# Optimization experiments

Hardware: AMD Instinct MI355X
Metric: run time of the kernel (lower is better)

## Reference

```python
import jax, jax.numpy as jnp
import numpy as np

ALG_DIM = 248   # dim of E8 adjoint rep
NNZ = 30000     # number of nonzero structure constants f_{ij}^k
BATCH = 8192


def setup_inputs() -> dict:
    key = jax.random.key(0)
    k1, k2, k3, k4, k5, k6 = jax.random.split(key, 6)
    x = jax.random.normal(k1, (BATCH, ALG_DIM), dtype=jnp.float32)
    y = jax.random.normal(k2, (BATCH, ALG_DIM), dtype=jnp.float32)
    idx_i = jax.random.randint(k3, (NNZ,), 0, ALG_DIM, dtype=jnp.int32)
    idx_j = jax.random.randint(k4, (NNZ,), 0, ALG_DIM, dtype=jnp.int32)
    idx_k = jax.random.randint(k5, (NNZ,), 0, ALG_DIM, dtype=jnp.int32)
    coeff = jax.random.normal(k6, (NNZ,), dtype=jnp.float32)
    alpha = jnp.ones((1,), dtype=jnp.float32)
    return {"x": x, "y": y, "idx_i": idx_i, "idx_j": idx_j,
            "idx_k": idx_k, "coeff": coeff, "alpha": alpha}


def reference(x, y, idx_i, idx_j, idx_k, coeff, alpha):
    # Sparse Lie bracket via structure-constant triples:
    #   out[b, k] = sum_{t : idx_k[t]==k} coeff[t] * x[b, idx_i[t]] * y[b, idx_j[t]]
    vals = x[:, idx_i] * y[:, idx_j] * coeff[None, :]          # (B, nnz)
    bracket = jnp.zeros_like(x).at[:, idx_k].add(vals)          # (B, 248)
    return alpha[0] * bracket
```

## Files before the change

kernel.cpp:

```cpp
#include <hip/hip_runtime.h>

#define ALG_DIM 248
#define ROWS 32
#define KSPLIT 4
#define KPB 62
#define PMAX 1024
#define CB 32
#define PLSTRIDE_B 3984
#define PLSTRIDE_DW 996

typedef __fp16 h2v __attribute__((ext_vector_type(2)));
union H2U { unsigned u; h2v h; };


__global__ void k_hist(const int* __restrict__ idx_k, int* __restrict__ hist, int nnz) {
    __shared__ int h[256];
    const int b = blockIdx.x, tid = threadIdx.x;
    h[tid] = 0;
    __syncthreads();
    const int chunk = (nnz + CB - 1) / CB;
    const int lo = b * chunk, hi = min(nnz, lo + chunk);
    for (int t = lo + tid; t < hi; t += 256)
        atomicAdd(&h[idx_k[t]], 1);
    __syncthreads();
    hist[b * 256 + tid] = h[tid];
}

__global__ void k_sort(const int* __restrict__ hist, int* __restrict__ meta,
                       int* __restrict__ perm, int* __restrict__ ssz,
                       int* __restrict__ coff, int* __restrict__ glim,
                       uint2* __restrict__ packedP) {
    __shared__ int sz[256];
    __shared__ int ssl[256];
    __shared__ int red[256];
    const int t = threadIdx.x;

    int tot = 0;
    for (int b = 0; b < CB; ++b) tot += hist[b * 256 + t];
    sz[t] = (t < ALG_DIM) ? tot : 0;
    __syncthreads();
    red[t] = sz[t];
    __syncthreads();
    for (int off = 128; off > 0; off >>= 1) {
        if (t < off) red[t] = max(red[t], red[t + off]);
        __syncthreads();
    }
    __shared__ int Ps;
    if (t == 0) {
        int P = (red[0] + 7) & ~7;
        P = max(P, 8);
        P = min(P, PMAX);
        meta[0] = P;
        Ps = P;
    }
    __syncthreads();
    const int stride = Ps + 8;

    int rank = 0, mysz = 0;
    if (t < ALG_DIM) {
        mysz = sz[t];
        for (int k = 0; k < ALG_DIM; ++k) {
            int s2 = sz[k];
            rank += (s2 > mysz) || (s2 == mysz && k < t);
        }
        perm[rank] = t;
        ssz[rank]  = mysz;
        ssl[rank]  = mysz;
        const int base = rank * stride;
        glim[t] = base + Ps;
        int run = base;
        for (int b = 0; b < CB; ++b) {
            coff[b * 256 + t] = run;
            run += hist[b * 256 + t];
        }
    }
    __syncthreads();
    if (t < ALG_DIM) {
        const int by = rank / KPB;
        const int L  = by * KPB + (((rank - by * KPB) >> 4) << 4);
        const int trip = (ssl[L] + 7) & ~7;
        const int base = rank * stride;
        for (int e = mysz; e < trip + 8; ++e)
            packedP[base + e] = make_uint2(0u, 0u);
    }
}

__global__ void k_scatter(const int* __restrict__ idx_i, const int* __restrict__ idx_j,
                          const int* __restrict__ idx_k, const float* __restrict__ coeff,
                          const int* __restrict__ coff, const int* __restrict__ glim,
                          uint2* __restrict__ packedP, int nnz) {
    __shared__ int cur[256];
    __shared__ int lim[256];
    const int b = blockIdx.x, tid = threadIdx.x;
    cur[tid] = coff[b * 256 + tid];
    lim[tid] = glim[tid];
    __syncthreads();
    const int chunk = (nnz + CB - 1) / CB;
    const int lo = b * chunk, hi = min(nnz, lo + chunk);
    for (int t = lo + tid; t < hi; t += 256) {
        const int k = idx_k[t];
        const int pos = atomicAdd(&cur[k], 1);
        if (pos < lim[k]) {
            const float c = coeff[t];
            H2U hc; hc.h = __builtin_amdgcn_cvt_pkrtz(c, c);
            uint2 p;
            p.x = ((unsigned)idx_i[t] << 4) | ((unsigned)idx_j[t] << 20);
            p.y = hc.u;
            packedP[pos] = p;
        }
    }
}


__global__ __launch_bounds__(256, 4) void k_main(
    const float* __restrict__ x, const float* __restrict__ y,
    const uint4* __restrict__ packed4,
    const int* __restrict__ meta, const int* __restrict__ perm,
    const int* __restrict__ ssz,
    const float* __restrict__ alpha_p, float* __restrict__ out)
{
    __shared__ __align__(16) unsigned xs32[4 * PLSTRIDE_DW];
    __shared__ __align__(16) unsigned ys32[4 * PLSTRIDE_DW];

    const int tid = threadIdx.x;
    const int r0  = blockIdx.x * ROWS;

    for (int u = tid; u < (ALG_DIM / 4) * (ROWS / 2); u += 256) {
        const int rp = u & 15;
        const int cq = u >> 4;
        const size_t ra = (size_t)(r0 + 2 * rp) * ALG_DIM + 4 * cq;
        const float4 xa = *reinterpret_cast<const float4*>(x + ra);
        const float4 xb = *reinterpret_cast<const float4*>(x + ra + ALG_DIM);
        const float4 ya = *reinterpret_cast<const float4*>(y + ra);
        const float4 yb = *reinterpret_cast<const float4*>(y + ra + ALG_DIM);
        const int pbase = (rp >> 2) * PLSTRIDE_DW + (rp & 3);
#define STG(d, XA, XB, YA, YB)                                                  \
        {                                                                       \
            const int dw = pbase + (4 * cq + (d)) * 4;                          \
            H2U hx; hx.h = __builtin_amdgcn_cvt_pkrtz(XA, XB);                  \
            H2U hy; hy.h = __builtin_amdgcn_cvt_pkrtz(YA, YB);                  \
            xs32[dw] = hx.u;                                                    \
            ys32[dw] = hy.u;                                                    \
        }
        STG(0, xa.x, xb.x, ya.x, yb.x)
        STG(1, xa.y, xb.y, ya.y, yb.y)
        STG(2, xa.z, xb.z, ya.z, yb.z)
        STG(3, xa.w, xb.w, ya.w, yb.w)
#undef STG
    }
    __syncthreads();

    const int   P     = meta[0];
    const float alpha = alpha_p[0];
    const int   S     = tid >> 2;
    const int   q     = tid & 3;

    const char* xsb = reinterpret_cast<const char*>(xs32) + q * PLSTRIDE_B;
    const char* ysb = reinterpret_cast<const char*>(ys32) + q * PLSTRIDE_B;

    if (S < KPB) {
        const int p = blockIdx.y * KPB + S;
        const int k = perm[p];

        const int pw   = blockIdx.y * KPB + ((tid >> 6) << 4);
        const int trip = __builtin_amdgcn_readfirstlane((ssz[pw] + 7) & ~7);
        const int nH   = trip >> 1;

        const uint4* tp = packed4 + (size_t)p * ((size_t)(P + 8) >> 1);

        float a0 = 0.f, a1 = 0.f, a2 = 0.f, a3 = 0.f,
              a4 = 0.f, a5 = 0.f, a6 = 0.f, a7 = 0.f;

        uint4 cur = tp[0];

#define PROC(PW, PC)                                                            \
        {                                                                       \
            const unsigned ox = (PW) & 0xFFFFu;                                 \
            const unsigned oy = (PW) >> 16;                                     \
            const uint4 wx = *reinterpret_cast<const uint4*>(xsb + ox);         \
            const uint4 wy = *reinterpret_cast<const uint4*>(ysb + oy);         \
            H2U cc; cc.u = (PC);                                                \
            H2U ux, uy;                                                         \
            ux.u = wx.x; uy.u = wy.x; c0 = (ux.h * uy.h) * cc.h + c0;           \
            ux.u = wx.y; uy.u = wy.y; c1 = (ux.h * uy.h) * cc.h + c1;           \
            ux.u = wx.z; uy.u = wy.z; c2 = (ux.h * uy.h) * cc.h + c2;           \
            ux.u = wx.w; uy.u = wy.w; c3 = (ux.h * uy.h) * cc.h + c3;           \
        }

        for (int chunk = 0; chunk < nH; chunk += 16) {
            h2v c0 = (h2v)0.0f, c1 = (h2v)0.0f, c2 = (h2v)0.0f, c3 = (h2v)0.0f;
            const int hend = min(chunk + 16, nH);
#pragma unroll 2
            for (int h = chunk; h < hend; ++h) {
                const uint4 nxt = tp[h + 1];
                PROC(cur.x, cur.y)
                PROC(cur.z, cur.w)
                cur = nxt;
            }
            a0 += (float)c0.x; a1 += (float)c0.y;
            a2 += (float)c1.x; a3 += (float)c1.y;
            a4 += (float)c2.x; a5 += (float)c2.y;
            a6 += (float)c3.x; a7 += (float)c3.y;
        }
#undef PROC

        const int rbase = r0 + (q << 3);
        out[(size_t)(rbase + 0) * ALG_DIM + k] = alpha * a0;
        out[(size_t)(rbase + 1) * ALG_DIM + k] = alpha * a1;
        out[(size_t)(rbase + 2) * ALG_DIM + k] = alpha * a2;
        out[(size_t)(rbase + 3) * ALG_DIM + k] = alpha * a3;
        out[(size_t)(rbase + 4) * ALG_DIM + k] = alpha * a4;
        out[(size_t)(rbase + 5) * ALG_DIM + k] = alpha * a5;
        out[(size_t)(rbase + 6) * ALG_DIM + k] = alpha * a6;
        out[(size_t)(rbase + 7) * ALG_DIM + k] = alpha * a7;
    }
}


extern "C" void kernel_launch(void* const* d_in, const int* in_sizes, int n_in,
                              void* d_out, int out_size, void* d_ws, size_t ws_size,
                              hipStream_t stream) {
    const float* x      = (const float*)d_in[0];
    const float* y      = (const float*)d_in[1];
    const int*   idx_i  = (const int*)d_in[2];
    const int*   idx_j  = (const int*)d_in[3];
    const int*   idx_k  = (const int*)d_in[4];
    const float* coeff  = (const float*)d_in[5];
    const float* alpha  = (const float*)d_in[6];
    float*       out    = (float*)d_out;

    const int nnz   = in_sizes[2];
    const int batch = in_sizes[0] / ALG_DIM;

    char*  ws      = (char*)d_ws;
    int*   meta    = (int*)ws;
    int*   perm    = (int*)(ws + 1024);
    int*   ssz     = (int*)(ws + 2048);
    int*   glim    = (int*)(ws + 3072);
    int*   hist    = (int*)(ws + 4096);
    int*   coff    = (int*)(ws + 4096 + CB * 256 * 4);
    uint2* packedP = (uint2*)(ws + 4096 + 2 * CB * 256 * 4 + 1024);

    k_hist   <<<CB, 256, 0, stream>>>(idx_k, hist, nnz);
    k_sort   <<<1, 256, 0, stream>>>(hist, meta, perm, ssz, coff, glim, packedP);
    k_scatter<<<CB, 256, 0, stream>>>(idx_i, idx_j, idx_k, coeff, coff, glim,
                                      packedP, nnz);

    dim3 grid(batch / ROWS, KSPLIT);
    k_main<<<grid, 256, 0, stream>>>(x, y, (const uint4*)packedP, meta, perm, ssz,
                                     alpha, out);
}
```

Before: 121.2 us.

## Fuse preprocessing and main phases into one cooperative persistent kernel

Measured after the change: 364.1 us. 3x slower.

```diff
diff --git a/kernel.cpp b/kernel.cpp
--- a/kernel.cpp
+++ b/kernel.cpp
@@ -1,4 +1,7 @@
 #include <hip/hip_runtime.h>
+#include <hip/hip_cooperative_groups.h>
+
+namespace cg = cooperative_groups;
 
 #define ALG_DIM 248
 #define ROWS 32
@@ -13,9 +16,9 @@
 union H2U { unsigned u; h2v h; };
 
 
-__global__ void k_hist(const int* __restrict__ idx_k, int* __restrict__ hist, int nnz) {
-    __shared__ int h[256];
-    const int b = blockIdx.x, tid = threadIdx.x;
+__device__ __forceinline__ void phase_hist(const int* __restrict__ idx_k,
+                                           int* __restrict__ hist, int nnz,
+                                           int b, int tid, int* h ) {
     h[tid] = 0;
     __syncthreads();
     const int chunk = (nnz + CB - 1) / CB;
@@ -26,56 +29,49 @@
     hist[b * 256 + tid] = h[tid];
 }
 
-__global__ void k_sort(const int* __restrict__ hist, int* __restrict__ meta,
-                       int* __restrict__ perm, int* __restrict__ ssz,
-                       int* __restrict__ coff, int* __restrict__ glim,
-                       uint2* __restrict__ packedP) {
-    __shared__ int sz[256];
-    __shared__ int ssl[256];
-    __shared__ int red[256];
-    const int t = threadIdx.x;
-
+__device__ __forceinline__ void phase_sort(const int* __restrict__ hist,
+                                           int* __restrict__ meta, int* __restrict__ perm,
+                                           int* __restrict__ ssz, int* __restrict__ coff,
+                                           int* __restrict__ glim, uint2* __restrict__ packedP,
+                                           int tid, int* sz ) {
+    int* ssl = sz + 256;
+    int* red = ssl + 256;
     int tot = 0;
-    for (int b = 0; b < CB; ++b) tot += hist[b * 256 + t];
-    sz[t] = (t < ALG_DIM) ? tot : 0;
-    __syncthreads();
-    red[t] = sz[t];
+    for (int b = 0; b < CB; ++b) tot += hist[b * 256 + tid];
+    sz[tid] = (tid < ALG_DIM) ? tot : 0;
+    __syncthreads();
+    red[tid] = sz[tid];
     __syncthreads();
     for (int off = 128; off > 0; off >>= 1) {
-        if (t < off) red[t] = max(red[t], red[t + off]);
+        if (tid < off) red[tid] = max(red[tid], red[tid + off]);
         __syncthreads();
     }
-    __shared__ int Ps;
-    if (t == 0) {
-        int P = (red[0] + 7) & ~7;
-        P = max(P, 8);
-        P = min(P, PMAX);
-        meta[0] = P;
-        Ps = P;
-    }
-    __syncthreads();
-    const int stride = Ps + 8;
+    int P = (red[0] + 7) & ~7;
+    P = max(P, 8);
+    P = min(P, PMAX);
+    if (tid == 0) meta[0] = P;
+    const int stride = P + 8;
 
     int rank = 0, mysz = 0;
-    if (t < ALG_DIM) {
-        mysz = sz[t];
+    if (tid < ALG_DIM) {
+        mysz = sz[tid];
         for (int k = 0; k < ALG_DIM; ++k) {
             int s2 = sz[k];
-            rank += (s2 > mysz) || (s2 == mysz && k < t);
-        }
-        perm[rank] = t;
+            rank += (s2 > mysz) || (s2 == mysz && k < tid);
+        }
+        perm[rank] = tid;
         ssz[rank]  = mysz;
         ssl[rank]  = mysz;
         const int base = rank * stride;
-        glim[t] = base + Ps;
+        glim[tid] = base + P;
         int run = base;
         for (int b = 0; b < CB; ++b) {
-            coff[b * 256 + t] = run;
-            run += hist[b * 256 + t];
-        }
-    }
-    __syncthreads();
-    if (t < ALG_DIM) {
+            coff[b * 256 + tid] = run;
+            run += hist[b * 256 + tid];
+        }
+    }
+    __syncthreads();
+    if (tid < ALG_DIM) {
         const int by = rank / KPB;
         const int L  = by * KPB + (((rank - by * KPB) >> 4) << 4);
         const int trip = (ssl[L] + 7) & ~7;
@@ -85,13 +81,15 @@
     }
 }
 
-__global__ void k_scatter(const int* __restrict__ idx_i, const int* __restrict__ idx_j,
-                          const int* __restrict__ idx_k, const float* __restrict__ coeff,
-                          const int* __restrict__ coff, const int* __restrict__ glim,
-                          uint2* __restrict__ packedP, int nnz) {
-    __shared__ int cur[256];
-    __shared__ int lim[256];
-    const int b = blockIdx.x, tid = threadIdx.x;
+__device__ __forceinline__ void phase_scatter(const int* __restrict__ idx_i,
+                                              const int* __restrict__ idx_j,
+                                              const int* __restrict__ idx_k,
+                                              const float* __restrict__ coeff,
+                                              const int* __restrict__ coff,
+                                              const int* __restrict__ glim,
+                                              uint2* __restrict__ packedP, int nnz,
+                                              int b, int tid, int* cur ) {
+    int* lim = cur + 256;
     cur[tid] = coff[b * 256 + tid];
     lim[tid] = glim[tid];
     __syncthreads();
@@ -111,19 +109,17 @@
     }
 }
 
-
-__global__ __launch_bounds__(256, 4) void k_main(
-    const float* __restrict__ x, const float* __restrict__ y,
-    const uint4* __restrict__ packed4,
-    const int* __restrict__ meta, const int* __restrict__ perm,
-    const int* __restrict__ ssz,
-    const float* __restrict__ alpha_p, float* __restrict__ out)
-{
-    __shared__ __align__(16) unsigned xs32[4 * PLSTRIDE_DW];
-    __shared__ __align__(16) unsigned ys32[4 * PLSTRIDE_DW];
-
-    const int tid = threadIdx.x;
-    const int r0  = blockIdx.x * ROWS;
+__device__ __forceinline__ void phase_main(const float* __restrict__ x,
+                                           const float* __restrict__ y,
+                                           const uint2* __restrict__ packedP,
+                                           const int* __restrict__ meta,
+                                           const int* __restrict__ perm,
+                                           const int* __restrict__ ssz,
+                                           float alpha, float* __restrict__ out,
+                                           int bx, int by, int tid,
+                                           unsigned* xs32 ) {
+    unsigned* ys32 = xs32 + 4 * PLSTRIDE_DW;
+    const int r0 = bx * ROWS;
 
     for (int u = tid; u < (ALG_DIM / 4) * (ROWS / 2); u += 256) {
         const int rp = u & 15;
@@ -150,23 +146,23 @@
     }
     __syncthreads();
 
-    const int   P     = meta[0];
-    const float alpha = alpha_p[0];
-    const int   S     = tid >> 2;
-    const int   q     = tid & 3;
+    const int P = meta[0];
+    const int S = tid >> 2;
+    const int q = tid & 3;
 
     const char* xsb = reinterpret_cast<const char*>(xs32) + q * PLSTRIDE_B;
-    const char* ysb = reinterpret_cast<const char*>(ys32) + q * PLSTRIDE_B;
+    const char* ysb = reinterpret_cast<const char*>(xs32 + 4 * PLSTRIDE_DW) + q * PLSTRIDE_B;
 
     if (S < KPB) {
-        const int p = blockIdx.y * KPB + S;
+        const int p = by * KPB + S;
         const int k = perm[p];
 
-        const int pw   = blockIdx.y * KPB + ((tid >> 6) << 4);
+        const int pw   = by * KPB + ((tid >> 6) << 4);
         const int trip = __builtin_amdgcn_readfirstlane((ssz[pw] + 7) & ~7);
         const int nH   = trip >> 1;
 
-        const uint4* tp = packed4 + (size_t)p * ((size_t)(P + 8) >> 1);
+        const uint4* tp = reinterpret_cast<const uint4*>(packedP)
+                        + (size_t)p * ((size_t)(P + 8) >> 1);
 
         float a0 = 0.f, a1 = 0.f, a2 = 0.f, a3 = 0.f,
               a4 = 0.f, a5 = 0.f, a6 = 0.f, a7 = 0.f;
@@ -186,12 +182,11 @@
             ux.u = wx.z; uy.u = wy.z; c2 = (ux.h * uy.h) * cc.h + c2;           \
             ux.u = wx.w; uy.u = wy.w; c3 = (ux.h * uy.h) * cc.h + c3;           \
         }
-
-        for (int chunk = 0; chunk < nH; chunk += 16) {
+        for (int ch = 0; ch < nH; ch += 16) {
             h2v c0 = (h2v)0.0f, c1 = (h2v)0.0f, c2 = (h2v)0.0f, c3 = (h2v)0.0f;
-            const int hend = min(chunk + 16, nH);
+            const int hend = min(ch + 16, nH);
 #pragma unroll 2
-            for (int h = chunk; h < hend; ++h) {
+            for (int h = ch; h < hend; ++h) {
                 const uint4 nxt = tp[h + 1];
                 PROC(cur.x, cur.y)
                 PROC(cur.z, cur.w)
@@ -214,6 +209,79 @@
         out[(size_t)(rbase + 6) * ALG_DIM + k] = alpha * a6;
         out[(size_t)(rbase + 7) * ALG_DIM + k] = alpha * a7;
     }
+}
+
+
+__global__ __launch_bounds__(256, 4) void k_all(
+    const float* __restrict__ x, const float* __restrict__ y,
+    const int* __restrict__ idx_i, const int* __restrict__ idx_j,
+    const int* __restrict__ idx_k, const float* __restrict__ coeff,
+    const float* __restrict__ alpha_p, float* __restrict__ out,
+    int* __restrict__ hist, int* __restrict__ meta, int* __restrict__ perm,
+    int* __restrict__ ssz, int* __restrict__ coff, int* __restrict__ glim,
+    uint2* __restrict__ packedP, int nnz, int batch)
+{
+    __shared__ __align__(16) char SMEM[8 * PLSTRIDE_DW * 4];
+    cg::grid_group gg = cg::this_grid();
+    const int tid = threadIdx.x;
+    const int gid = blockIdx.x;
+
+    if (gid < CB)
+        phase_hist(idx_k, hist, nnz, gid, tid, (int*)SMEM);
+    gg.sync();
+
+    if (gid == 0)
+        phase_sort(hist, meta, perm, ssz, coff, glim, packedP, tid, (int*)SMEM);
+    gg.sync();
+
+    if (gid < CB)
+        phase_scatter(idx_i, idx_j, idx_k, coeff, coff, glim, packedP, nnz,
+                      gid, tid, (int*)SMEM);
+    gg.sync();
+
+    const float alpha = alpha_p[0];
+    const int nxb = batch / ROWS;
+    const int ntiles = nxb * KSPLIT;
+    for (int tile = gid; tile < ntiles; tile += gridDim.x) {
+        __syncthreads();
+        phase_main(x, y, packedP, meta, perm, ssz, alpha, out,
+                   tile % nxb, tile / nxb, tid, (unsigned*)SMEM);
+    }
+}
+
+
+__global__ void k_hist_f(const int* __restrict__ idx_k, int* __restrict__ hist, int nnz) {
+    __shared__ int h[256];
+    phase_hist(idx_k, hist, nnz, blockIdx.x, threadIdx.x, h);
+}
+
+__global__ void k_sort_f(const int* __restrict__ hist, int* __restrict__ meta,
+                         int* __restrict__ perm, int* __restrict__ ssz,
+                         int* __restrict__ coff, int* __restrict__ glim,
+                         uint2* __restrict__ packedP) {
+    __shared__ int sz[768];
+    phase_sort(hist, meta, perm, ssz, coff, glim, packedP, threadIdx.x, sz);
+}
+
+__global__ void k_scatter_f(const int* __restrict__ idx_i, const int* __restrict__ idx_j,
+                            const int* __restrict__ idx_k, const float* __restrict__ coeff,
+                            const int* __restrict__ coff, const int* __restrict__ glim,
+                            uint2* __restrict__ packedP, int nnz) {
+    __shared__ int cur[512];
+    phase_scatter(idx_i, idx_j, idx_k, coeff, coff, glim, packedP, nnz,
+                  blockIdx.x, threadIdx.x, cur);
+}
+
+__global__ __launch_bounds__(256, 4) void k_main_f(
+    const float* __restrict__ x, const float* __restrict__ y,
+    const uint2* __restrict__ packedP,
+    const int* __restrict__ meta, const int* __restrict__ perm,
+    const int* __restrict__ ssz,
+    const float* __restrict__ alpha_p, float* __restrict__ out)
+{
+    __shared__ __align__(16) unsigned SM[8 * PLSTRIDE_DW];
+    phase_main(x, y, packedP, meta, perm, ssz, alpha_p[0], out,
+               blockIdx.x, blockIdx.y, threadIdx.x, SM);
 }
 
 
@@ -229,8 +297,8 @@
     const float* alpha  = (const float*)d_in[6];
     float*       out    = (float*)d_out;
 
-    const int nnz   = in_sizes[2];
-    const int batch = in_sizes[0] / ALG_DIM;
+    int nnz   = in_sizes[2];
+    int batch = in_sizes[0] / ALG_DIM;
 
     char*  ws      = (char*)d_ws;
     int*   meta    = (int*)ws;
@@ -241,12 +309,31 @@
     int*   coff    = (int*)(ws + 4096 + CB * 256 * 4);
     uint2* packedP = (uint2*)(ws + 4096 + 2 * CB * 256 * 4 + 1024);
 
-    k_hist   <<<CB, 256, 0, stream>>>(idx_k, hist, nnz);
-    k_sort   <<<1, 256, 0, stream>>>(hist, meta, perm, ssz, coff, glim, packedP);
-    k_scatter<<<CB, 256, 0, stream>>>(idx_i, idx_j, idx_k, coeff, coff, glim,
-                                      packedP, nnz);
-
-    dim3 grid(batch / ROWS, KSPLIT);
-    k_main<<<grid, 256, 0, stream>>>(x, y, (const uint4*)packedP, meta, perm, ssz,
-                                     alpha, out);
-}
+    const int ntiles = (batch / ROWS) * KSPLIT;
+
+    int dev = 0;
+    (void)hipGetDevice(&dev);
+    int numCU = 0, maxb = 0;
+    (void)hipDeviceGetAttribute(&numCU, hipDeviceAttributeMultiprocessorCount, dev);
+    (void)hipOccupancyMaxActiveBlocksPerMultiprocessor(&maxb, (const void*)k_all, 256, 0);
+
+    hipError_t err = hipErrorUnknown;
+    if (numCU > 0 && maxb > 0) {
+        int grid = maxb * numCU;
+        if (grid > ntiles) grid = ntiles;
+        void* args[] = { &x, &y, &idx_i, &idx_j, &idx_k, &coeff, &alpha, &out,
+                         &hist, &meta, &perm, &ssz, &coff, &glim, &packedP,
+                         &nnz, &batch };
+        err = hipLaunchCooperativeKernel((const void*)k_all, dim3(grid), dim3(256),
+                                         args, 0, stream);
+    }
+
+    if (err != hipSuccess) {
+        k_hist_f   <<<CB, 256, 0, stream>>>(idx_k, hist, nnz);
+        k_sort_f   <<<1, 256, 0, stream>>>(hist, meta, perm, ssz, coff, glim, packedP);
+        k_scatter_f<<<CB, 256, 0, stream>>>(idx_i, idx_j, idx_k, coeff, coff, glim,
+                                            packedP, nnz);
+        dim3 grid(batch / ROWS, KSPLIT);
+        k_main_f<<<grid, 256, 0, stream>>>(x, y, packedP, meta, perm, ssz, alpha, out);
+    }
+}
```
